# Kernel optimization log

Hardware: AMD Instinct MI355X
Metric: run time of the kernel (lower is better)

Reference implementation:

```python
import jax, jax.numpy as jnp
import numpy as np
from jax import lax

B, T_MEL, M = 4, 63, 80
HOP, K_UP, WIN = 256, 800, 1024
R, S, Q = 120, 240, 256
NB, K, CYCLE = 16, 2, 8
PAD_UP = (K_UP + 4 * HOP - WIN) // 2  # 400
L = (T_MEL - 1) * HOP  # 15872


def conv1d(x, w, b, dilation=1, pad=(0, 0)):
    # x: [B,Cin,L], w: [Cout,Cin,K]
    y = lax.conv_general_dilated(x, w, (1,), [pad], rhs_dilation=(dilation,),
                                 dimension_numbers=('NCH', 'OIH', 'NCH'))
    return y + b[None, :, None]


def setup_inputs() -> dict:
    key = jax.random.key(0)
    ks = jax.random.split(key, 20)
    rn = lambda k, shape, s=0.05: (jax.random.normal(k, shape, jnp.float32) * s)
    return {
        'waveforms': jax.random.normal(ks[0], (B, L), jnp.float32),
        'melspecs': jax.random.normal(ks[1], (B, M, T_MEL), jnp.float32),
        # ConvTranspose1d weight, torch layout (in, out, k)
        'w_up': rn(ks[2], (M, M, K_UP)), 'b_up': rn(ks[3], (M,)),
        'w_in': rn(ks[4], (R, 1, 1)), 'b_in': rn(ks[5], (R,)),
        # per-block params stacked on leading axis
        'w_gate': rn(ks[6], (NB, 2 * R, R, K)), 'b_gate': rn(ks[7], (NB, 2 * R)),
        'w_cond': rn(ks[8], (NB, 2 * R, M, 1)), 'b_cond': rn(ks[9], (NB, 2 * R)),
        'w_res': rn(ks[10], (NB, R, R, 1)), 'b_res': rn(ks[11], (NB, R)),
        'w_skip': rn(ks[12], (NB, S, R, 1)), 'b_skip': rn(ks[13], (NB, S)),
        'w_h1': rn(ks[14], (Q, S, 1)), 'b_h1': rn(ks[15], (Q,)),
        'w_h2': rn(ks[16], (Q, Q, 1)), 'b_h2': rn(ks[17], (Q,)),
    }


def reference(waveforms, melspecs, w_up, b_up, w_in, b_in, w_gate, b_gate,
              w_cond, b_cond, w_res, b_res, w_skip, b_skip, w_h1, b_h1, w_h2, b_h2):
    # upsample = ConvTranspose1d: lhs-dilated conv with flipped, transposed kernel
    wt = jnp.flip(jnp.transpose(w_up, (1, 0, 2)), -1)  # [out,in,k]
    p = K_UP - 1 - PAD_UP  # 399
    conditions = lax.conv_general_dilated(
        melspecs, wt, (1,), [(p, p)], lhs_dilation=(HOP,),
        dimension_numbers=('NCH', 'OIH', 'NCH')) + b_up[None, :, None]

    length = min(waveforms.shape[-1], conditions.shape[-1])
    wav = waveforms[..., :length]
    cond = conditions[..., :length]

    residuals = conv1d(wav[:, None, :], w_in, b_in)  # [B,R,L]
    skips = jnp.zeros((wav.shape[0], S, length), residuals.dtype)
    for i in range(NB):
        d = 2 ** (i % CYCLE)
        gated = conv1d(residuals, w_gate[i], b_gate[i], dilation=d, pad=((K - 1) * d, 0))
        gated = gated + conv1d(cond, w_cond[i], b_cond[i])
        f, g = jnp.split(gated, 2, axis=1)
        z = jnp.tanh(f) * jax.nn.sigmoid(g)  # [B,R,L]
        skips = skips + conv1d(z, w_skip[i], b_skip[i])
        residuals = residuals + conv1d(z, w_res[i], b_res[i])

    h = conv1d(jax.nn.relu(skips), w_h1, b_h1)
    logits = conv1d(jax.nn.relu(h), w_h2, b_h2)  # [B,Q,L]
    return logits
```

## Files before the change

kernel.cpp:

```cpp
#include <hip/hip_runtime.h>
#include <math.h>

#define B_   4
#define M_   80
#define TMEL 63
#define R_   120
#define S_   240
#define Q_   256
#define NB_  16
#define L_   15872

typedef float  f32x4  __attribute__((ext_vector_type(4)));
typedef short  bf16x8 __attribute__((ext_vector_type(8)));
typedef short  short4_t __attribute__((ext_vector_type(4)));

__device__ __forceinline__ short f2bf(float x) {
  unsigned u = __builtin_bit_cast(unsigned, x);
  u += 0x7fffu + ((u >> 16) & 1u);
  return (short)(u >> 16);
}
__device__ __forceinline__ float bf2f(unsigned short s) {
  unsigned u = ((unsigned)s) << 16;
  return __builtin_bit_cast(float, u);
}

__global__ __launch_bounds__(256) void prep_melT_kernel(
    const float* __restrict__ mel, short* __restrict__ melT)
{
  const int idx = blockIdx.x * 256 + threadIdx.x;
  if (idx >= B_ * TMEL * M_) return;
  const int m = idx % M_;
  const int i = (idx / M_) % TMEL;
  const int b = idx / (M_ * TMEL);
  melT[idx] = f2bf(mel[b * (M_ * TMEL) + m * TMEL + i]);
}

__global__ __launch_bounds__(256) void prep_wup_kernel(
    const float* __restrict__ w_up, short* __restrict__ Wup)
{
  __shared__ float T[M_][65];
  const int c  = blockIdx.x >> 4;
  const int j  = (blockIdx.x >> 2) & 3;
  const int fb = blockIdx.x & 3;
  for (int idx = threadIdx.x; idx < M_ * 64; idx += 256) {
    const int pl = idx & 63, m = idx >> 6;
    const int phi = fb * 64 + pl;
    const int dmin = (phi < 112) ? -1 : -2;
    const int dmax = (phi < 144) ? 1 : 0;
    const int delta = dmin + j;
    float v = 0.0f;
    if (delta <= dmax)
      v = w_up[m * (M_ * 800) + c * 800 + (400 + phi + 256 * delta)];
    T[m][pl] = v;
  }
  __syncthreads();
  for (int idx = threadIdx.x; idx < 64 * M_; idx += 256) {
    const int m = idx % M_, pl = idx / M_;
    const int phi = fb * 64 + pl;
    Wup[((size_t)phi * M_ + c) * 320 + j * 80 + m] = f2bf(T[m][pl]);
  }
}

#define KPU 328

__global__ __launch_bounds__(256, 2) void upsample_mfma_kernel(
    const short* __restrict__ melT, const short* __restrict__ Wup,
    const float* __restrict__ b_up, short* __restrict__ condb)
{
  __shared__ __align__(16) short Xu[64 * KPU];
  const int tid = threadIdx.x;
  const int phi = blockIdx.x;
  const int r0 = blockIdx.y * 64;
  const int dmin = (phi < 112) ? -1 : -2;

  for (int idx = tid; idx < 2560; idx += 256) {
    const int v = idx % 10;
    const int j = (idx / 10) & 3;
    const int rl = idx / 40;
    const int rho = r0 + rl;
    const int b = rho / 62;
    const int n = rho - b * 62;
    const int i = n - (dmin + j);
    int4 val = make_int4(0, 0, 0, 0);
    if (b < B_ && i >= 0 && i < TMEL)
      val = *(const int4*)&melT[((size_t)b * TMEL + i) * M_ + v * 8];
    *(int4*)&Xu[rl * KPU + j * 80 + v * 8] = val;
  }
  __syncthreads();

  const int lane = tid & 63;
  const int wv = tid >> 6;
  const int col = lane & 15;
  const int quad = lane >> 4;
  const int kq = quad * 8;

  f32x4 acc[5];
#pragma unroll
  for (int i = 0; i < 5; ++i) acc[i] = (f32x4)(0.f);
#pragma unroll
  for (int ks = 0; ks < 10; ++ks) {
    bf16x8 a = *(const bf16x8*)&Xu[(wv * 16 + col) * KPU + ks * 32 + kq];
#pragma unroll
    for (int ct = 0; ct < 5; ++ct) {
      bf16x8 b = *(const bf16x8*)(Wup + ((size_t)phi * M_ + ct * 16 + col) * 320 + ks * 32 + kq);
      acc[ct] = __builtin_amdgcn_mfma_f32_16x16x32_bf16(a, b, acc[ct], 0, 0, 0);
    }
  }
#pragma unroll
  for (int ct = 0; ct < 5; ++ct) {
    const int c = ct * 16 + col;
    const float bc = b_up[c];
#pragma unroll
    for (int reg = 0; reg < 4; ++reg) {
      const int rho = r0 + wv * 16 + quad * 4 + reg;
      if (rho < 248) {
        const int b = rho / 62;
        const int n = rho - b * 62;
        const int t = phi + (n << 8);
        condb[((size_t)b * L_ + t) * M_ + c] = f2bf(acc[ct][reg] + bc);
      }
    }
  }
}

__global__ __launch_bounds__(256) void in_conv_kernel(
    const float* __restrict__ wav, const float* __restrict__ w_in,
    const float* __restrict__ b_in, short* __restrict__ res)
{
  const int idx = blockIdx.x * 256 + threadIdx.x;
  const int r = idx & 127;
  const int rem = idx >> 7;
  const int t = rem % L_;
  const int b = rem / L_;
  res[idx] = (r < R_) ? f2bf(w_in[r] * wav[b * L_ + t] + b_in[r]) : (short)0;
}

__global__ __launch_bounds__(256) void prepack_w1_kernel(
    const float* __restrict__ wg, const float* __restrict__ wc,
    short* __restrict__ W1p)
{
  const int idx = blockIdx.x * 256 + threadIdx.x;
  const int k = idx % 320;
  const int cp = (idx / 320) % 256;
  const int i = idx / (320 * 256);
  int corig = -1;
  if (cp < 128) { if (cp < 120) corig = cp; }
  else          { const int c = cp - 128; if (c < 120) corig = 120 + c; }
  float val = 0.0f;
  if (corig >= 0) {
    if (k < 120)      val = wg[((size_t)(i * 240 + corig) * 120 + k) * 2 + 0];
    else if (k < 240) val = wg[((size_t)(i * 240 + corig) * 120 + (k - 120)) * 2 + 1];
    else              val = wc[(size_t)(i * 240 + corig) * 80 + (k - 240)];
  }
  W1p[idx] = f2bf(val);
}

__global__ __launch_bounds__(256) void prepack_w2_kernel(
    const float* __restrict__ wsk, const float* __restrict__ wr,
    short* __restrict__ W2p)
{
  const int idx = blockIdx.x * 256 + threadIdx.x;
  const int k = idx % 128;
  const int sp = (idx / 128) % 384;
  const int i = idx / (128 * 384);
  float val = 0.0f;
  if (k < 120) {
    if (sp < 240)      val = wsk[(size_t)(i * 240 + sp) * 120 + k];
    else if (sp < 360) val = wr[(size_t)(i * 120 + (sp - 240)) * 120 + k];
  }
  W2p[idx] = f2bf(val);
}

__global__ __launch_bounds__(256) void prepack_rest_kernel(
    const float* __restrict__ wh1, const float* __restrict__ wh2,
    const float* __restrict__ bg, const float* __restrict__ bc,
    const float* __restrict__ bs, const float* __restrict__ br,
    short* __restrict__ Wh1p, short* __restrict__ Wh2p,
    float* __restrict__ bias1p, float* __restrict__ bias2p)
{
  const int idx = blockIdx.x * 256 + threadIdx.x;
  if (idx < 65536) {
    const int q = idx >> 8, k = idx & 255;
    Wh1p[idx] = f2bf(k < 240 ? wh1[q * 240 + k] : 0.0f);
  } else if (idx < 131072) {
    Wh2p[idx - 65536] = f2bf(wh2[idx - 65536]);
  } else if (idx < 135168) {
    const int j = idx - 131072;
    const int i = j >> 8, cp = j & 255;
    float v = 0.0f;
    if (cp < 128) { if (cp < 120) v = bg[i * 240 + cp] + bc[i * 240 + cp]; }
    else { const int c = cp - 128; if (c < 120) v = bg[i * 240 + 120 + c] + bc[i * 240 + 120 + c]; }
    bias1p[j] = v;
  } else if (idx < 141312) {
    const int j = idx - 135168;
    const int i = j / 384, sp = j % 384;
    float v = 0.0f;
    if (sp < 240)      v = bs[i * 240 + sp];
    else if (sp < 360) v = br[i * 120 + (sp - 240)];
    bias2p[j] = v;
  }
}

#define KP1 320
#define SGP 248
#define NTILE (L_ / 64)
#define NWG   (NTILE * B_)
#define CPX   (NWG / 8)

__device__ __forceinline__ int xswz(int row, int k) {
  return row * KP1 + (k ^ ((row & 7) << 3));
}

__global__ __launch_bounds__(512, 4) void block_mfma_kernel(
    const short* __restrict__ res_in, short* __restrict__ res_out,
    unsigned short* __restrict__ skips, const short* __restrict__ condb,
    const short* __restrict__ W1, const short* __restrict__ W2,
    const float* __restrict__ bias1, const float* __restrict__ bias2,
    const int d, const int first)
{
  __shared__ __align__(16) short Xs[64 * KP1];

  const int tid = threadIdx.x;
  const int w_id = blockIdx.y * NTILE + blockIdx.x;
  const int nid  = (w_id & 7) * CPX + (w_id >> 3);
  const int bb   = nid / NTILE;
  const int t0   = (nid - bb * NTILE) * 64;

  {
    const int dd = (d <= 64) ? d : 64;
    const int nr = 64 + dd;
    for (int idx = tid; idx < nr * 15; idx += 512) {
      const int rr = idx / 15, c8 = idx - rr * 15;
      int ts;
      if (d <= 64)      ts = t0 - d + rr;
      else              ts = (rr < 64) ? (t0 - 128 + rr) : (t0 + rr - 64);
      int4 v = make_int4(0, 0, 0, 0);
      if (ts >= 0)
        v = *(const int4*)(res_in + ((size_t)(bb * L_ + ts) * 128 + c8 * 8));
      if (rr < 64)
        *(int4*)&Xs[xswz(rr, c8 * 8)] = v;
      const int r1 = rr - dd;
      if (r1 >= 0)
        *(int4*)&Xs[xswz(r1, 120 + c8 * 8)] = v;
    }
  }
  for (int idx = tid; idx < 640; idx += 512) {
    const int c = idx % 10, trw = idx / 10;
    const int4 v = *(const int4*)(condb + ((size_t)(bb * L_ + t0 + trw) * M_ + c * 8));
    *(int4*)&Xs[xswz(trw, 240 + c * 8)] = v;
  }
  __syncthreads();

  const int lane = tid & 63;
  const int wv = tid >> 6;
  const int col = lane & 15;
  const int quad = lane >> 4;
  const int kq = quad * 8;

  f32x4 acc[4][2];
#pragma unroll
  for (int a = 0; a < 4; ++a)
#pragma unroll
    for (int b = 0; b < 2; ++b) acc[a][b] = (f32x4)(0.f);
  __builtin_amdgcn_s_setprio(1);
#pragma unroll
  for (int ks = 0; ks < 10; ++ks) {
    bf16x8 av[4];
#pragma unroll
    for (int tf = 0; tf < 4; ++tf)
      av[tf] = *(const bf16x8*)&Xs[xswz(tf * 16 + col, ks * 32 + kq)];
#pragma unroll
    for (int ct = 0; ct < 2; ++ct) {
      const int cpt = ((ct == 0) ? wv : (wv + 8)) * 16 + col;
      bf16x8 b = *(const bf16x8*)(W1 + cpt * 320 + ks * 32 + kq);
#pragma unroll
      for (int tf = 0; tf < 4; ++tf)
        acc[tf][ct] = __builtin_amdgcn_mfma_f32_16x16x32_bf16(av[tf], b, acc[tf][ct], 0, 0, 0);
    }
  }
  __builtin_amdgcn_s_setprio(0);

  __syncthreads();

  {
    const int ch = wv * 16 + col;
    if (ch < 120) {
      const float bf_ = bias1[ch];
      const float bg_ = bias1[128 + ch];
#pragma unroll
      for (int tf = 0; tf < 4; ++tf) {
#pragma unroll
        for (int reg = 0; reg < 4; ++reg) {
          float f = acc[tf][0][reg] + bf_;
          float g = acc[tf][1][reg] + bg_;
          f = fminf(fmaxf(f, -15.f), 15.f);
          g = fminf(fmaxf(g, -15.f), 15.f);
          const float ef = __expf(2.0f * f);
          const float th = (ef - 1.0f) * __builtin_amdgcn_rcpf(ef + 1.0f);
          const float eg = __expf(-g);
          const float sg = __builtin_amdgcn_rcpf(1.0f + eg);
          const int t = tf * 16 + quad * 4 + reg;
          Xs[xswz(t, ch)] = f2bf(th * sg);
        }
      }
    }
  }
  if (tid < 64)
    *(int4*)&Xs[xswz(tid, 240)] = make_int4(0, 0, 0, 0);
  __syncthreads();

  const size_t srow = ((size_t)bb * L_ + t0) * 240;
  int4 sk0 = make_int4(0,0,0,0), sk1 = sk0, sk2 = sk0, sk3 = sk0;
  if (!first) {
    {
      const int idx = tid;
      const int row = idx / 30, j = idx - row * 30;
      sk0 = *(const int4*)(skips + srow + row * 240 + j * 8);
    }
    {
      const int idx = tid + 512;
      const int row = idx / 30, j = idx - row * 30;
      sk1 = *(const int4*)(skips + srow + row * 240 + j * 8);
    }
    {
      const int idx = tid + 1024;
      const int row = idx / 30, j = idx - row * 30;
      sk2 = *(const int4*)(skips + srow + row * 240 + j * 8);
    }
    if (tid + 1536 < 1920) {
      const int idx = tid + 1536;
      const int row = idx / 30, j = idx - row * 30;
      sk3 = *(const int4*)(skips + srow + row * 240 + j * 8);
    }
  }

  f32x4 acc2[4][3];
#pragma unroll
  for (int a = 0; a < 4; ++a)
#pragma unroll
    for (int b = 0; b < 3; ++b) acc2[a][b] = (f32x4)(0.f);
  __builtin_amdgcn_s_setprio(1);
#pragma unroll
  for (int ks = 0; ks < 4; ++ks) {
    const int ko = ks * 32 + kq;
    const int kz = (ko >= 120) ? (ko + 120) : ko;
    bf16x8 av[4];
#pragma unroll
    for (int tf = 0; tf < 4; ++tf)
      av[tf] = *(const bf16x8*)&Xs[xswz(tf * 16 + col, kz)];
#pragma unroll
    for (int st = 0; st < 3; ++st) {
      bf16x8 b = *(const bf16x8*)(W2 + ((wv * 3 + st) * 16 + col) * 128 + ks * 32 + kq);
#pragma unroll
      for (int tf = 0; tf < 4; ++tf)
        acc2[tf][st] = __builtin_amdgcn_mfma_f32_16x16x32_bf16(av[tf], b, acc2[tf][st], 0, 0, 0);
    }
  }
  __builtin_amdgcn_s_setprio(0);

  if (wv >= 5) {
#pragma unroll
    for (int st = 0; st < 3; ++st) {
      const int tile = wv * 3 + st;
      if (tile < 23) {
        const int s = tile * 16 + col;
        const int r = s - 240;
        if (r < 120) {
          const float b2 = bias2[s];
#pragma unroll
          for (int tf = 0; tf < 4; ++tf) {
#pragma unroll
            for (int reg = 0; reg < 4; ++reg) {
              const int t = tf * 16 + quad * 4 + reg;
              const float old = bf2f((unsigned short)Xs[xswz(t, 120 + r)]);
              res_out[((size_t)(bb * L_ + t0 + t)) * 128 + r] =
                  f2bf(old + acc2[tf][st][reg] + b2);
            }
          }
        }
      }
    }
  }
  __syncthreads();

  short* SG = Xs;
  if (wv < 5) {
#pragma unroll
    for (int st = 0; st < 3; ++st) {
      const int tile = wv * 3 + st;
      const int s = tile * 16 + col;
      const float b2 = bias2[s];
#pragma unroll
      for (int tf = 0; tf < 4; ++tf)
#pragma unroll
        for (int reg = 0; reg < 4; ++reg)
          SG[(tf * 16 + quad * 4 + reg) * SGP + s] = f2bf(acc2[tf][st][reg] + b2);
    }
  }
  __syncthreads();

  {
#pragma unroll
    for (int it = 0; it < 4; ++it) {
      const int idx = tid + it * 512;
      if (idx < 1920) {
        const int row = idx / 30;
        const int j = idx - row * 30;
        unsigned short* gp = skips + srow + row * 240 + j * 8;
        int4 sv = *(const int4*)&SG[row * SGP + j * 8];
        const unsigned short* svp = (const unsigned short*)&sv;
        float vals[8];
#pragma unroll
        for (int e = 0; e < 8; ++e) vals[e] = bf2f(svp[e]);
        if (!first) {
          const int4 ov = (it == 0) ? sk0 : (it == 1) ? sk1 : (it == 2) ? sk2 : sk3;
          const unsigned short* ovp = (const unsigned short*)&ov;
#pragma unroll
          for (int e = 0; e < 8; ++e) vals[e] += bf2f(ovp[e]);
        }
        int4 res;
        unsigned short* rp = (unsigned short*)&res;
#pragma unroll
        for (int e = 0; e < 8; ++e) rp[e] = (unsigned short)f2bf(vals[e]);
        *(int4*)gp = res;
      }
    }
  }
}

#define KPH 264

__global__ __launch_bounds__(256, 2) void head_mfma_kernel(
    const unsigned short* __restrict__ skips,
    const short* __restrict__ Wh1, const short* __restrict__ Wh2,
    const float* __restrict__ bh1, const float* __restrict__ bh2,
    float* __restrict__ out)
{
  __shared__ __align__(16) short Ss[64 * KPH];
  short* const Hs = Ss;

  const int tid = threadIdx.x;
  const int w_id = blockIdx.y * NTILE + blockIdx.x;
  const int nid  = (w_id & 7) * CPX + (w_id >> 3);
  const int bb   = nid / NTILE;
  const int t0   = (nid - bb * NTILE) * 64;

  for (int idx = tid; idx < 2048; idx += 256) {
    const int c = idx & 31, trw = idx >> 5;
    if (c < 30) {
      int4 v = *(const int4*)(skips + ((size_t)(bb * L_ + t0 + trw) * 240 + c * 8));
      int* vi = (int*)&v;
#pragma unroll
      for (int j = 0; j < 4; ++j) {
        unsigned x = (unsigned)vi[j];
        unsigned lo = x & 0xFFFFu; if (lo & 0x8000u) lo = 0;
        unsigned hi = x >> 16;     if (hi & 0x8000u) hi = 0;
        vi[j] = (int)(lo | (hi << 16));
      }
      *(int4*)&Ss[trw * KPH + c * 8] = v;
    } else {
      *(int4*)&Ss[trw * KPH + c * 8] = make_int4(0, 0, 0, 0);
    }
  }
  __syncthreads();

  const int lane = tid & 63;
  const int wv = tid >> 6;
  const int col = lane & 15;
  const int quad = lane >> 4;
  const int kq = quad * 8;

  f32x4 acc[4][4];
#pragma unroll
  for (int a = 0; a < 4; ++a)
#pragma unroll
    for (int b = 0; b < 4; ++b) acc[a][b] = (f32x4)(0.f);
#pragma unroll
  for (int ks = 0; ks < 8; ++ks) {
    bf16x8 av[4];
#pragma unroll
    for (int tf = 0; tf < 4; ++tf)
      av[tf] = *(const bf16x8*)&Ss[(tf * 16 + col) * KPH + ks * 32 + kq];
#pragma unroll
    for (int ct = 0; ct < 4; ++ct) {
      bf16x8 b = *(const bf16x8*)(Wh1 + ((wv * 4 + ct) * 16 + col) * 256 + ks * 32 + kq);
#pragma unroll
      for (int tf = 0; tf < 4; ++tf)
        acc[tf][ct] = __builtin_amdgcn_mfma_f32_16x16x32_bf16(av[tf], b, acc[tf][ct], 0, 0, 0);
    }
  }

  __syncthreads();

#pragma unroll
  for (int ct = 0; ct < 4; ++ct) {
    const int q = (wv * 4 + ct) * 16 + col;
    const float b1 = bh1[q];
#pragma unroll
    for (int tf = 0; tf < 4; ++tf)
#pragma unroll
      for (int reg = 0; reg < 4; ++reg)
        Hs[(tf * 16 + quad * 4 + reg) * KPH + q] = f2bf(fmaxf(acc[tf][ct][reg] + b1, 0.0f));
  }
  __syncthreads();

  f32x4 acc2[4][4];
#pragma unroll
  for (int a = 0; a < 4; ++a)
#pragma unroll
    for (int b = 0; b < 4; ++b) acc2[a][b] = (f32x4)(0.f);
#pragma unroll
  for (int ks = 0; ks < 8; ++ks) {
    bf16x8 av[4];
#pragma unroll
    for (int tf = 0; tf < 4; ++tf)
      av[tf] = *(const bf16x8*)&Hs[(tf * 16 + col) * KPH + ks * 32 + kq];
#pragma unroll
    for (int ct = 0; ct < 4; ++ct) {
      bf16x8 b = *(const bf16x8*)(Wh2 + ((wv * 4 + ct) * 16 + col) * 256 + ks * 32 + kq);
#pragma unroll
      for (int tf = 0; tf < 4; ++tf)
        acc2[tf][ct] = __builtin_amdgcn_mfma_f32_16x16x32_bf16(av[tf], b, acc2[tf][ct], 0, 0, 0);
    }
  }
#pragma unroll
  for (int ct = 0; ct < 4; ++ct) {
    const int q = (wv * 4 + ct) * 16 + col;
    const float b2 = bh2[q];
#pragma unroll
    for (int tf = 0; tf < 4; ++tf) {
      const int tg0 = t0 + tf * 16 + quad * 4;
      float4 o = make_float4(acc2[tf][ct][0] + b2, acc2[tf][ct][1] + b2,
                             acc2[tf][ct][2] + b2, acc2[tf][ct][3] + b2);
      *(float4*)(out + ((size_t)(bb * Q_ + q)) * L_ + tg0) = o;
    }
  }
}

extern "C" void kernel_launch(void* const* d_in, const int* in_sizes, int n_in,
                              void* d_out, int out_size, void* d_ws, size_t ws_size,
                              hipStream_t stream) {
  const float* wav    = (const float*)d_in[0];
  const float* mel    = (const float*)d_in[1];
  const float* w_up   = (const float*)d_in[2];
  const float* b_up   = (const float*)d_in[3];
  const float* w_in   = (const float*)d_in[4];
  const float* b_in   = (const float*)d_in[5];
  const float* w_gate = (const float*)d_in[6];
  const float* b_gate = (const float*)d_in[7];
  const float* w_cond = (const float*)d_in[8];
  const float* b_cond = (const float*)d_in[9];
  const float* w_res  = (const float*)d_in[10];
  const float* b_res  = (const float*)d_in[11];
  const float* w_skip = (const float*)d_in[12];
  const float* b_skip = (const float*)d_in[13];
  const float* w_h1   = (const float*)d_in[14];
  const float* b_h1   = (const float*)d_in[15];
  const float* w_h2   = (const float*)d_in[16];
  const float* b_h2   = (const float*)d_in[17];
  float* out = (float*)d_out;

  char* w = (char*)d_ws;
  short* condb   = (short*)w;                 w += (size_t)B_ * L_ * M_ * 2;
  short* res0    = (short*)w;                 w += (size_t)B_ * L_ * 128 * 2;
  short* res1    = (short*)w;                 w += (size_t)B_ * L_ * 128 * 2;
  unsigned short* skips = (unsigned short*)w; w += (size_t)B_ * L_ * 240 * 2;
  short* W1p     = (short*)w;                 w += (size_t)16 * 256 * 320 * 2;
  short* W2p     = (short*)w;                 w += (size_t)16 * 384 * 128 * 2;
  short* Wh1p    = (short*)w;                 w += (size_t)256 * 256 * 2;
  short* Wh2p    = (short*)w;                 w += (size_t)256 * 256 * 2;
  float* bias1p  = (float*)w;                 w += (size_t)16 * 256 * 4;
  float* bias2p  = (float*)w;                 w += (size_t)16 * 384 * 4;
  short* melT    = (short*)w;                 w += (size_t)B_ * TMEL * M_ * 2;
  short* Wup = (short*)skips;

  prepack_w1_kernel<<<(16 * 256 * 320) / 256, 256, 0, stream>>>(w_gate, w_cond, W1p);
  prepack_w2_kernel<<<(16 * 384 * 128) / 256, 256, 0, stream>>>(w_skip, w_res, W2p);
  prepack_rest_kernel<<<141312 / 256, 256, 0, stream>>>(
      w_h1, w_h2, b_gate, b_cond, b_skip, b_res, Wh1p, Wh2p, bias1p, bias2p);
  prep_melT_kernel<<<(B_ * TMEL * M_ + 255) / 256, 256, 0, stream>>>(mel, melT);
  prep_wup_kernel<<<80 * 4 * 4, 256, 0, stream>>>(w_up, Wup);

  dim3 ugrid(256, 4);
  upsample_mfma_kernel<<<ugrid, 256, 0, stream>>>(melT, Wup, b_up, condb);
  in_conv_kernel<<<((size_t)B_ * L_ * 128) / 256, 256, 0, stream>>>(wav, w_in, b_in, res0);

  dim3 bgrid(L_ / 64, B_);
  for (int i = 0; i < NB_; ++i) {
    const int d = 1 << (i & 7);
    const short* rin  = (i & 1) ? res1 : res0;
    short*       rout = (i & 1) ? res0 : res1;
    block_mfma_kernel<<<bgrid, 512, 0, stream>>>(
        rin, rout, skips, condb,
        W1p + (size_t)i * 256 * 320, W2p + (size_t)i * 384 * 128,
        bias1p + i * 256, bias2p + i * 384,
        d, (i == 0) ? 1 : 0);
  }

  head_mfma_kernel<<<bgrid, 256, 0, stream>>>(skips, Wh1p, Wh2p, b_h1, b_h2, out);
}
```

Measured before the change: 1.016 ms.

## Fuse last WaveNet block with output head into one kernel

The final residual block is moved into a dedicated kernel that skips the unneeded residual output, accumulates the skip sum in LDS, applies ReLU, and runs both head 1x1 convs in place. This removes one kernel launch and a full write then re-read of the bf16 skips tensor, and drops the residual output write of the last block. The head now runs with 512 threads per 64-step tile, which changes the work per wave and the register pressure. The hardcoded dilation 128 for block 15 matches 2^(15%8).

```diff
diff --git a/kernel.cpp b/kernel.cpp
--- a/kernel.cpp
+++ b/kernel.cpp
@@ -203,6 +203,7 @@
 
 #define KP1 320
 #define SGP 248
+#define SGP2 264
 #define NTILE (L_ / 64)
 #define NWG   (NTILE * B_)
 #define CPX   (NWG / 8)
@@ -279,7 +280,6 @@
     }
   }
   __builtin_amdgcn_s_setprio(0);
-
   __syncthreads();
 
   {
@@ -312,26 +312,15 @@
   const size_t srow = ((size_t)bb * L_ + t0) * 240;
   int4 sk0 = make_int4(0,0,0,0), sk1 = sk0, sk2 = sk0, sk3 = sk0;
   if (!first) {
-    {
-      const int idx = tid;
-      const int row = idx / 30, j = idx - row * 30;
-      sk0 = *(const int4*)(skips + srow + row * 240 + j * 8);
-    }
-    {
-      const int idx = tid + 512;
-      const int row = idx / 30, j = idx - row * 30;
-      sk1 = *(const int4*)(skips + srow + row * 240 + j * 8);
-    }
-    {
-      const int idx = tid + 1024;
-      const int row = idx / 30, j = idx - row * 30;
-      sk2 = *(const int4*)(skips + srow + row * 240 + j * 8);
-    }
+    { const int idx = tid;        const int row = idx / 30, j = idx - row * 30;
+      sk0 = *(const int4*)(skips + srow + row * 240 + j * 8); }
+    { const int idx = tid + 512;  const int row = idx / 30, j = idx - row * 30;
+      sk1 = *(const int4*)(skips + srow + row * 240 + j * 8); }
+    { const int idx = tid + 1024; const int row = idx / 30, j = idx - row * 30;
+      sk2 = *(const int4*)(skips + srow + row * 240 + j * 8); }
     if (tid + 1536 < 1920) {
-      const int idx = tid + 1536;
-      const int row = idx / 30, j = idx - row * 30;
-      sk3 = *(const int4*)(skips + srow + row * 240 + j * 8);
-    }
+      const int idx = tid + 1536; const int row = idx / 30, j = idx - row * 30;
+      sk3 = *(const int4*)(skips + srow + row * 240 + j * 8); }
   }
 
   f32x4 acc2[4][3];
@@ -399,45 +388,43 @@
   }
   __syncthreads();
 
-  {
-#pragma unroll
-    for (int it = 0; it < 4; ++it) {
-      const int idx = tid + it * 512;
-      if (idx < 1920) {
-        const int row = idx / 30;
-        const int j = idx - row * 30;
-        unsigned short* gp = skips + srow + row * 240 + j * 8;
-        int4 sv = *(const int4*)&SG[row * SGP + j * 8];
-        const unsigned short* svp = (const unsigned short*)&sv;
-        float vals[8];
-#pragma unroll
-        for (int e = 0; e < 8; ++e) vals[e] = bf2f(svp[e]);
-        if (!first) {
-          const int4 ov = (it == 0) ? sk0 : (it == 1) ? sk1 : (it == 2) ? sk2 : sk3;
-          const unsigned short* ovp = (const unsigned short*)&ov;
-#pragma unroll
-          for (int e = 0; e < 8; ++e) vals[e] += bf2f(ovp[e]);
-        }
-        int4 res;
-        unsigned short* rp = (unsigned short*)&res;
-#pragma unroll
-        for (int e = 0; e < 8; ++e) rp[e] = (unsigned short)f2bf(vals[e]);
-        *(int4*)gp = res;
+#pragma unroll
+  for (int it = 0; it < 4; ++it) {
+    const int idx = tid + it * 512;
+    if (idx < 1920) {
+      const int row = idx / 30;
+      const int j = idx - row * 30;
+      unsigned short* gp = skips + srow + row * 240 + j * 8;
+      int4 sv = *(const int4*)&SG[row * SGP + j * 8];
+      const unsigned short* svp = (const unsigned short*)&sv;
+      float vals[8];
+#pragma unroll
+      for (int e = 0; e < 8; ++e) vals[e] = bf2f(svp[e]);
+      if (!first) {
+        const int4 ov = (it == 0) ? sk0 : (it == 1) ? sk1 : (it == 2) ? sk2 : sk3;
+        const unsigned short* ovp = (const unsigned short*)&ov;
+#pragma unroll
+        for (int e = 0; e < 8; ++e) vals[e] += bf2f(ovp[e]);
       }
-    }
-  }
-}
-
-#define KPH 264
-
-__global__ __launch_bounds__(256, 2) void head_mfma_kernel(
-    const unsigned short* __restrict__ skips,
+      int4 res;
+      unsigned short* rp = (unsigned short*)&res;
+#pragma unroll
+      for (int e = 0; e < 8; ++e) rp[e] = (unsigned short)f2bf(vals[e]);
+      *(int4*)gp = res;
+    }
+  }
+}
+
+__global__ __launch_bounds__(512, 4) void block_mfma_last_kernel(
+    const short* __restrict__ res_in,
+    const unsigned short* __restrict__ skips, const short* __restrict__ condb,
+    const short* __restrict__ W1, const short* __restrict__ W2,
+    const float* __restrict__ bias1, const float* __restrict__ bias2,
     const short* __restrict__ Wh1, const short* __restrict__ Wh2,
     const float* __restrict__ bh1, const float* __restrict__ bh2,
     float* __restrict__ out)
 {
-  __shared__ __align__(16) short Ss[64 * KPH];
-  short* const Hs = Ss;
+  __shared__ __align__(16) short Xs[64 * KP1];
 
   const int tid = threadIdx.x;
   const int w_id = blockIdx.y * NTILE + blockIdx.x;
@@ -445,22 +432,22 @@
   const int bb   = nid / NTILE;
   const int t0   = (nid - bb * NTILE) * 64;
 
-  for (int idx = tid; idx < 2048; idx += 256) {
-    const int c = idx & 31, trw = idx >> 5;
-    if (c < 30) {
-      int4 v = *(const int4*)(skips + ((size_t)(bb * L_ + t0 + trw) * 240 + c * 8));
-      int* vi = (int*)&v;
-#pragma unroll
-      for (int j = 0; j < 4; ++j) {
-        unsigned x = (unsigned)vi[j];
-        unsigned lo = x & 0xFFFFu; if (lo & 0x8000u) lo = 0;
-        unsigned hi = x >> 16;     if (hi & 0x8000u) hi = 0;
-        vi[j] = (int)(lo | (hi << 16));
-      }
-      *(int4*)&Ss[trw * KPH + c * 8] = v;
-    } else {
-      *(int4*)&Ss[trw * KPH + c * 8] = make_int4(0, 0, 0, 0);
-    }
+  for (int idx = tid; idx < 128 * 15; idx += 512) {
+    const int rr = idx / 15, c8 = idx - rr * 15;
+    const int ts = (rr < 64) ? (t0 - 128 + rr) : (t0 + rr - 64);
+    int4 v = make_int4(0, 0, 0, 0);
+    if (ts >= 0)
+      v = *(const int4*)(res_in + ((size_t)(bb * L_ + ts) * 128 + c8 * 8));
+    if (rr < 64)
+      *(int4*)&Xs[xswz(rr, c8 * 8)] = v;
+    const int r1 = rr - 64;
+    if (r1 >= 0)
+      *(int4*)&Xs[xswz(r1, 120 + c8 * 8)] = v;
+  }
+  for (int idx = tid; idx < 640; idx += 512) {
+    const int c = idx % 10, trw = idx / 10;
+    const int4 v = *(const int4*)(condb + ((size_t)(bb * L_ + t0 + trw) * M_ + c * 8));
+    *(int4*)&Xs[xswz(trw, 240 + c * 8)] = v;
   }
   __syncthreads();
 
@@ -470,68 +457,203 @@
   const int quad = lane >> 4;
   const int kq = quad * 8;
 
-  f32x4 acc[4][4];
+  f32x4 acc[4][2];
 #pragma unroll
   for (int a = 0; a < 4; ++a)
 #pragma unroll
-    for (int b = 0; b < 4; ++b) acc[a][b] = (f32x4)(0.f);
+    for (int b = 0; b < 2; ++b) acc[a][b] = (f32x4)(0.f);
+  __builtin_amdgcn_s_setprio(1);
+#pragma unroll
+  for (int ks = 0; ks < 10; ++ks) {
+    bf16x8 av[4];
+#pragma unroll
+    for (int tf = 0; tf < 4; ++tf)
+      av[tf] = *(const bf16x8*)&Xs[xswz(tf * 16 + col, ks * 32 + kq)];
+#pragma unroll
+    for (int ct = 0; ct < 2; ++ct) {
+      const int cpt = ((ct == 0) ? wv : (wv + 8)) * 16 + col;
+      bf16x8 b = *(const bf16x8*)(W1 + cpt * 320 + ks * 32 + kq);
+#pragma unroll
+      for (int tf = 0; tf < 4; ++tf)
+        acc[tf][ct] = __builtin_amdgcn_mfma_f32_16x16x32_bf16(av[tf], b, acc[tf][ct], 0, 0, 0);
+    }
+  }
+  __builtin_amdgcn_s_setprio(0);
+  __syncthreads();
+
+  {
+    const int ch = wv * 16 + col;
+    if (ch < 120) {
+      const float bf_ = bias1[ch];
+      const float bg_ = bias1[128 + ch];
+#pragma unroll
+      for (int tf = 0; tf < 4; ++tf) {
+#pragma unroll
+        for (int reg = 0; reg < 4; ++reg) {
+          float f = acc[tf][0][reg] + bf_;
+          float g = acc[tf][1][reg] + bg_;
+          f = fminf(fmaxf(f, -15.f), 15.f);
+          g = fminf(fmaxf(g, -15.f), 15.f);
+          const float ef = __expf(2.0f * f);
+          const float th = (ef - 1.0f) * __builtin_amdgcn_rcpf(ef + 1.0f);
+          const float eg = __expf(-g);
+          const float sg = __builtin_amdgcn_rcpf(1.0f + eg);
+          const int t = tf * 16 + quad * 4 + reg;
+          Xs[xswz(t, ch)] = f2bf(th * sg);
+        }
+      }
+    }
+  }
+  if (tid < 64)
+    *(int4*)&Xs[xswz(tid, 240)] = make_int4(0, 0, 0, 0);
+  __syncthreads();
+
+  const size_t srow = ((size_t)bb * L_ + t0) * 240;
+  int4 sk0, sk1, sk2, sk3 = make_int4(0,0,0,0);
+  { const int idx = tid;        const int row = idx / 30, j = idx - row * 30;
+    sk0 = *(const int4*)(skips + srow + row * 240 + j * 8); }
+  { const int idx = tid + 512;  const int row = idx / 30, j = idx - row * 30;
+    sk1 = *(const int4*)(skips + srow + row * 240 + j * 8); }
+  { const int idx = tid + 1024; const int row = idx / 30, j = idx - row * 30;
+    sk2 = *(const int4*)(skips + srow + row * 240 + j * 8); }
+  if (tid + 1536 < 1920) {
+    const int idx = tid + 1536; const int row = idx / 30, j = idx - row * 30;
+    sk3 = *(const int4*)(skips + srow + row * 240 + j * 8); }
+
+  f32x4 acc2[4][2];
+#pragma unroll
+  for (int a = 0; a < 4; ++a)
+#pragma unroll
+    for (int b = 0; b < 2; ++b) acc2[a][b] = (f32x4)(0.f);
+  __builtin_amdgcn_s_setprio(1);
+#pragma unroll
+  for (int ks = 0; ks < 4; ++ks) {
+    const int ko = ks * 32 + kq;
+    const int kz = (ko >= 120) ? (ko + 120) : ko;
+    bf16x8 av[4];
+#pragma unroll
+    for (int tf = 0; tf < 4; ++tf)
+      av[tf] = *(const bf16x8*)&Xs[xswz(tf * 16 + col, kz)];
+#pragma unroll
+    for (int st = 0; st < 2; ++st) {
+      const int tile = wv * 2 + st;
+      if (tile < 15) {
+        bf16x8 b = *(const bf16x8*)(W2 + (tile * 16 + col) * 128 + ks * 32 + kq);
+#pragma unroll
+        for (int tf = 0; tf < 4; ++tf)
+          acc2[tf][st] = __builtin_amdgcn_mfma_f32_16x16x32_bf16(av[tf], b, acc2[tf][st], 0, 0, 0);
+      }
+    }
+  }
+  __builtin_amdgcn_s_setprio(0);
+  __syncthreads();
+
+  short* SG = Xs;
+#pragma unroll
+  for (int st = 0; st < 2; ++st) {
+    const int tile = wv * 2 + st;
+    if (tile < 15) {
+      const int s = tile * 16 + col;
+      const float b2 = bias2[s];
+#pragma unroll
+      for (int tf = 0; tf < 4; ++tf)
+#pragma unroll
+        for (int reg = 0; reg < 4; ++reg)
+          SG[(tf * 16 + quad * 4 + reg) * SGP2 + s] = f2bf(acc2[tf][st][reg] + b2);
+    }
+  }
+  if (tid < 128) {
+    const int row = tid >> 1, g = tid & 1;
+    *(int4*)&SG[row * SGP2 + 240 + g * 8] = make_int4(0, 0, 0, 0);
+  }
+  __syncthreads();
+
+#pragma unroll
+  for (int it = 0; it < 4; ++it) {
+    const int idx = tid + it * 512;
+    if (idx < 1920) {
+      const int row = idx / 30;
+      const int j = idx - row * 30;
+      short* lp = &SG[row * SGP2 + j * 8];
+      int4 sv = *(const int4*)lp;
+      const unsigned short* svp = (const unsigned short*)&sv;
+      const int4 ov = (it == 0) ? sk0 : (it == 1) ? sk1 : (it == 2) ? sk2 : sk3;
+      const unsigned short* ovp = (const unsigned short*)&ov;
+      int4 res;
+      unsigned short* rp = (unsigned short*)&res;
+#pragma unroll
+      for (int e = 0; e < 8; ++e)
+        rp[e] = (unsigned short)f2bf(fmaxf(bf2f(svp[e]) + bf2f(ovp[e]), 0.0f));
+      *(int4*)lp = res;
+    }
+  }
+  __syncthreads();
+
+  f32x4 acc1[4][2];
+#pragma unroll
+  for (int a = 0; a < 4; ++a)
+#pragma unroll
+    for (int b = 0; b < 2; ++b) acc1[a][b] = (f32x4)(0.f);
+  __builtin_amdgcn_s_setprio(1);
 #pragma unroll
   for (int ks = 0; ks < 8; ++ks) {
     bf16x8 av[4];
 #pragma unroll
     for (int tf = 0; tf < 4; ++tf)
-      av[tf] = *(const bf16x8*)&Ss[(tf * 16 + col) * KPH + ks * 32 + kq];
-#pragma unroll
-    for (int ct = 0; ct < 4; ++ct) {
-      bf16x8 b = *(const bf16x8*)(Wh1 + ((wv * 4 + ct) * 16 + col) * 256 + ks * 32 + kq);
+      av[tf] = *(const bf16x8*)&SG[(tf * 16 + col) * SGP2 + ks * 32 + kq];
+#pragma unroll
+    for (int ct = 0; ct < 2; ++ct) {
+      bf16x8 b = *(const bf16x8*)(Wh1 + ((wv * 2 + ct) * 16 + col) * 256 + ks * 32 + kq);
 #pragma unroll
       for (int tf = 0; tf < 4; ++tf)
-        acc[tf][ct] = __builtin_amdgcn_mfma_f32_16x16x32_bf16(av[tf], b, acc[tf][ct], 0, 0, 0);
-    }
-  }
-
-  __syncthreads();
-
-#pragma unroll
-  for (int ct = 0; ct < 4; ++ct) {
-    const int q = (wv * 4 + ct) * 16 + col;
+        acc1[tf][ct] = __builtin_amdgcn_mfma_f32_16x16x32_bf16(av[tf], b, acc1[tf][ct], 0, 0, 0);
+    }
+  }
+  __builtin_amdgcn_s_setprio(0);
+  __syncthreads();
+
+#pragma unroll
+  for (int ct = 0; ct < 2; ++ct) {
+    const int q = (wv * 2 + ct) * 16 + col;
     const float b1 = bh1[q];
 #pragma unroll
     for (int tf = 0; tf < 4; ++tf)
 #pragma unroll
       for (int reg = 0; reg < 4; ++reg)
-        Hs[(tf * 16 + quad * 4 + reg) * KPH + q] = f2bf(fmaxf(acc[tf][ct][reg] + b1, 0.0f));
-  }
-  __syncthreads();
-
-  f32x4 acc2[4][4];
+        SG[(tf * 16 + quad * 4 + reg) * SGP2 + q] = f2bf(fmaxf(acc1[tf][ct][reg] + b1, 0.0f));
+  }
+  __syncthreads();
+
+  f32x4 acc2h[4][2];
 #pragma unroll
   for (int a = 0; a < 4; ++a)
 #pragma unroll
-    for (int b = 0; b < 4; ++b) acc2[a][b] = (f32x4)(0.f);
+    for (int b = 0; b < 2; ++b) acc2h[a][b] = (f32x4)(0.f);
+  __builtin_amdgcn_s_setprio(1);
 #pragma unroll
   for (int ks = 0; ks < 8; ++ks) {
     bf16x8 av[4];
 #pragma unroll
     for (int tf = 0; tf < 4; ++tf)
-      av[tf] = *(const bf16x8*)&Hs[(tf * 16 + col) * KPH + ks * 32 + kq];
-#pragma unroll
-    for (int ct = 0; ct < 4; ++ct) {
-      bf16x8 b = *(const bf16x8*)(Wh2 + ((wv * 4 + ct) * 16 + col) * 256 + ks * 32 + kq);
+      av[tf] = *(const bf16x8*)&SG[(tf * 16 + col) * SGP2 + ks * 32 + kq];
+#pragma unroll
+    for (int ct = 0; ct < 2; ++ct) {
+      bf16x8 b = *(const bf16x8*)(Wh2 + ((wv * 2 + ct) * 16 + col) * 256 + ks * 32 + kq);
 #pragma unroll
       for (int tf = 0; tf < 4; ++tf)
-        acc2[tf][ct] = __builtin_amdgcn_mfma_f32_16x16x32_bf16(av[tf], b, acc2[tf][ct], 0, 0, 0);
-    }
-  }
-#pragma unroll
-  for (int ct = 0; ct < 4; ++ct) {
-    const int q = (wv * 4 + ct) * 16 + col;
+        acc2h[tf][ct] = __builtin_amdgcn_mfma_f32_16x16x32_bf16(av[tf], b, acc2h[tf][ct], 0, 0, 0);
+    }
+  }
+  __builtin_amdgcn_s_setprio(0);
+#pragma unroll
+  for (int ct = 0; ct < 2; ++ct) {
+    const int q = (wv * 2 + ct) * 16 + col;
     const float b2 = bh2[q];
 #pragma unroll
     for (int tf = 0; tf < 4; ++tf) {
       const int tg0 = t0 + tf * 16 + quad * 4;
-      float4 o = make_float4(acc2[tf][ct][0] + b2, acc2[tf][ct][1] + b2,
-                             acc2[tf][ct][2] + b2, acc2[tf][ct][3] + b2);
+      float4 o = make_float4(acc2h[tf][ct][0] + b2, acc2h[tf][ct][1] + b2,
+                             acc2h[tf][ct][2] + b2, acc2h[tf][ct][3] + b2);
       *(float4*)(out + ((size_t)(bb * Q_ + q)) * L_ + tg0) = o;
     }
   }
@@ -585,8 +707,8 @@
   upsample_mfma_kernel<<<ugrid, 256, 0, stream>>>(melT, Wup, b_up, condb);
   in_conv_kernel<<<((size_t)B_ * L_ * 128) / 256, 256, 0, stream>>>(wav, w_in, b_in, res0);
 
-  dim3 bgrid(L_ / 64, B_);
-  for (int i = 0; i < NB_; ++i) {
+  dim3 bgrid(NTILE, B_);
+  for (int i = 0; i < NB_ - 1; ++i) {
     const int d = 1 << (i & 7);
     const short* rin  = (i & 1) ? res1 : res0;
     short*       rout = (i & 1) ? res0 : res1;
@@ -596,6 +718,9 @@
         bias1p + i * 256, bias2p + i * 384,
         d, (i == 0) ? 1 : 0);
   }
-
-  head_mfma_kernel<<<bgrid, 256, 0, stream>>>(skips, Wh1p, Wh2p, b_h1, b_h2, out);
-}
+  block_mfma_last_kernel<<<bgrid, 512, 0, stream>>>(
+      res1, skips, condb,
+      W1p + (size_t)15 * 256 * 320, W2p + (size_t)15 * 384 * 128,
+      bias1p + 15 * 256, bias2p + 15 * 384,
+      Wh1p, Wh2p, b_h1, b_h2, out);
+}
```

Result: faster. 994.3 us (-2.1%).
